# Kernel optimization log

Measured on AMD Instinct MI355X. Metric: run time of the kernel, lower is better.

## Reference

```python
import jax, jax.numpy as jnp
import numpy as np
from jax import lax

B = 32768        # batch
L = 1024         # input_size
K = 5            # kernel_size
PAD = K - 1      # circular padding = 4
FEA = L + (PAD - K // 2) * 2   # mem_fea_dim = 1028
MEM_DIM = 50
DATE_DIM = 32
SHRINK = 0.0025
EPS = 1e-12
DN = ('NCH', 'OIH', 'NCH')


def setup_inputs() -> dict:
    key = jax.random.key(0)
    ks = jax.random.split(key, 10)
    s = 0.05
    return {
        'x': jax.random.normal(ks[0], (B, L), jnp.float32),
        'date_vector': jax.random.normal(ks[1], (B, DATE_DIM), jnp.float32),
        'conv_w': jax.random.normal(ks[2], (1, 1, K), jnp.float32) * s,    # Conv1d weight [out,in,k]
        'convt_w': jax.random.normal(ks[3], (1, 1, K), jnp.float32) * s,   # ConvTranspose1d weight
        'mem_W': jax.random.normal(ks[4], (MEM_DIM, FEA), jnp.float32) * s,      # memory bank (codebook)
        'date_W': jax.random.normal(ks[5], (MEM_DIM, DATE_DIM), jnp.float32) * s, # date addressing weights
        'fcw_w': jax.random.normal(ks[6], (1, L), jnp.float32) * s,
        'fcw_b': jnp.zeros((1,), jnp.float32),
        'fcb_w': jax.random.normal(ks[7], (1, L), jnp.float32) * s,
        'fcb_b': jnp.zeros((1,), jnp.float32),
    }


def _forward(x, date_vector, conv_w, convt_w, mem_W, date_W, fcw_w, fcw_b, fcb_w, fcb_b):
    # --- encode: 1-channel circular conv (bias forced to 0 in original forward) ---
    st = x[:, None, :]                                            # [B,1,L]
    stp = jnp.pad(st, ((0, 0), (0, 0), (PAD, PAD)), mode='wrap')  # circular pad
    st = lax.conv_general_dilated(stp, conv_w, (1,), 'VALID', dimension_numbers=DN)  # [B,1,FEA]

    # --- DateMemoryUnit: date-addressed read with hard shrink + L1 renorm ---
    scores = date_vector @ date_W.T                               # [B,MEM_DIM]
    att = jax.nn.softmax(scores, axis=-1)
    att = jax.nn.relu(att - SHRINK) * att / (jnp.abs(att - SHRINK) + EPS)
    att = att / (jnp.sum(jnp.abs(att), axis=-1, keepdims=True) + EPS)
    st_mem = att @ mem_W                                          # [B,FEA]
    st = st_mem.reshape(B, 1, FEA)

    # --- decode: ConvTranspose1d(k=5, stride=1, padding=4) == VALID conv with flipped kernel ---
    st = lax.conv_general_dilated(st, jnp.flip(convt_w, -1), (1,), 'VALID', dimension_numbers=DN)
    st = st[:, 0, :]                                              # [B,L]

    # --- trend blend ---
    mtf = 0.5
    weight = jnp.tanh(x @ fcw_w.T + fcw_b) * mtf + 1.0            # [B,1]
    bias = jnp.tanh(x @ fcb_w.T + fcb_b) * mtf                    # [B,1]
    st = st * weight + bias
    return st, weight, bias


def reference(x, date_vector, conv_w, convt_w, mem_W, date_W, fcw_w, fcw_b, fcb_w, fcb_b):
    return _forward(x, date_vector, conv_w, convt_w, mem_W, date_W, fcw_w, fcw_b, fcb_w, fcb_b)
```

## Files before the change

### kernel.cpp

```cpp
#include <hip/hip_runtime.h>
#include <hip/hip_bf16.h>

#define BB   32768
#define LL   1024
#define FEA  1028
#define MEM  50
#define DATE 32

typedef float  f32x4  __attribute__((ext_vector_type(4)));
typedef __bf16 bf16x8 __attribute__((ext_vector_type(8)));

__device__ __forceinline__ float wave_max(float v) {
    #pragma unroll
    for (int off = 32; off; off >>= 1) v = fmaxf(v, __shfl_xor(v, off));
    return v;
}
__device__ __forceinline__ float wave_sum(float v) {
    #pragma unroll
    for (int off = 32; off; off >>= 1) v += __shfl_xor(v, off);
    return v;
}
__device__ __forceinline__ float fast_tanh(float v) {
    float e = __expf(2.f * v);
    return 1.f - 2.f / (e + 1.f);
}

__global__ __launch_bounds__(256) void prep_and_wb(
        const float* __restrict__ convt_w,
        const float* __restrict__ mem_W,
        const float* __restrict__ x,
        const float* __restrict__ fcw_w, const float* __restrict__ fcw_b,
        const float* __restrict__ fcb_w, const float* __restrict__ fcb_b,
        __bf16* __restrict__ wc,
        float* __restrict__ out) {
    if (blockIdx.x >= 2048) {
        int idx = (blockIdx.x - 2048) * 256 + threadIdx.x;
        int n = idx >> 6, k = idx & 63;
        float acc = 0.f;
        if (k < MEM) {
            #pragma unroll
            for (int j = 0; j < 5; ++j)
                acc += convt_w[j] * mem_W[k * FEA + n + 4 - j];
        }
        wc[n * 64 + k] = (__bf16)acc;
        return;
    }

    const int lane = threadIdx.x & 63;
    const int wid  = threadIdx.x >> 6;
    const int b0   = blockIdx.x * 16;

    f32x4 wv[4], bv[4];
    #pragma unroll
    for (int c = 0; c < 4; ++c) {
        wv[c] = *(const f32x4*)(fcw_w + c * 256 + lane * 4);
        bv[c] = *(const f32x4*)(fcb_w + c * 256 + lane * 4);
    }
    f32x4 xv[4][4];
    #pragma unroll
    for (int rr = 0; rr < 4; ++rr)
        #pragma unroll
        for (int c = 0; c < 4; ++c)
            xv[rr][c] = *(const f32x4*)(x + (size_t)(b0 + wid * 4 + rr) * LL
                                          + c * 256 + lane * 4);
    float fwb = fcw_b[0], fbb = fcb_b[0];
    #pragma unroll
    for (int rr = 0; rr < 4; ++rr) {
        int r = wid * 4 + rr;
        float aw = 0.f, ab = 0.f;
        #pragma unroll
        for (int c = 0; c < 4; ++c)
            #pragma unroll
            for (int j = 0; j < 4; ++j) {
                aw += xv[rr][c][j] * wv[c][j];
                ab += xv[rr][c][j] * bv[c][j];
            }
        #pragma unroll
        for (int off = 1; off <= 32; off <<= 1) {
            aw += __shfl_xor(aw, off);
            ab += __shfl_xor(ab, off);
        }
        if (lane == 0) {
            out[(size_t)BB * LL + (b0 + r)]      = fast_tanh(aw + fwb) * 0.5f + 1.0f;
            out[(size_t)BB * LL + BB + (b0 + r)] = fast_tanh(ab + fbb) * 0.5f;
        }
    }
}

__global__ __launch_bounds__(256) void memconv_main(
        const float* __restrict__ dv,
        const float* __restrict__ dW,
        const __bf16* __restrict__ wc,
        float* __restrict__ out) {
    __shared__ __bf16 att_s[16 * 72];
    __shared__ float  w_s[16], b_s[16];
    __shared__ float  stage[4][16 * 72];

    const int lane = threadIdx.x & 63;
    const int wid  = threadIdx.x >> 6;
    const int cg   = lane & 15;
    const int kg   = lane >> 4;
    const int b0   = blockIdx.x * 16;

    if (threadIdx.x < 16) {
        w_s[threadIdx.x] = out[(size_t)BB * LL + b0 + threadIdx.x];
        b_s[threadIdx.x] = out[(size_t)BB * LL + BB + b0 + threadIdx.x];
    }

    {
        int m = lane < MEM ? lane : MEM - 1;
        float dwv[DATE];
        const f32x4* dwp = (const f32x4*)(dW + m * DATE);
        #pragma unroll
        for (int c = 0; c < 8; ++c) {
            f32x4 v = dwp[c];
            #pragma unroll
            for (int j = 0; j < 4; ++j) dwv[c * 4 + j] = v[j];
        }
        #pragma unroll
        for (int rr = 0; rr < 4; ++rr) {
            int r = wid * 4 + rr;
            const f32x4* dvp = (const f32x4*)(dv + (size_t)(b0 + r) * DATE);
            float sc = 0.f;
            #pragma unroll
            for (int c = 0; c < 8; ++c) {
                f32x4 v = dvp[c];
                #pragma unroll
                for (int j = 0; j < 4; ++j) sc += v[j] * dwv[c * 4 + j];
            }
            float scm = (lane < MEM) ? sc : -1e30f;
            float mx  = wave_max(scm);
            float e   = (lane < MEM) ? __expf(sc - mx) : 0.f;
            float s   = wave_sum(e);
            float p   = e / s;
            float d   = p - 0.0025f;
            float p2  = (d > 0.f) ? p * d / (d + 1e-12f) : 0.f;
            float s2  = wave_sum(p2) + 1e-12f;
            float att = p2 / s2;
            att_s[r * 72 + lane] = (lane < MEM) ? (__bf16)att : (__bf16)0.f;
        }
    }
    __syncthreads();

    {
        bf16x8 bfr0 = *(const bf16x8*)(att_s + cg * 72 + kg * 8);
        bf16x8 bfr1 = *(const bf16x8*)(att_s + cg * 72 + 32 + kg * 8);
        float* st = stage[wid];
        const int n0 = wid * 256;
        #pragma unroll
        for (int R = 0; R < 4; ++R) {
            #pragma unroll
            for (int t = 0; t < 4; ++t) {
                int n = n0 + (R * 4 + t) * 16 + cg;
                bf16x8 a0 = *(const bf16x8*)(wc + n * 64 + kg * 8);
                bf16x8 a1 = *(const bf16x8*)(wc + n * 64 + 32 + kg * 8);
                f32x4 acc = {0.f, 0.f, 0.f, 0.f};
                acc = __builtin_amdgcn_mfma_f32_16x16x32_bf16(a0, bfr0, acc, 0, 0, 0);
                acc = __builtin_amdgcn_mfma_f32_16x16x32_bf16(a1, bfr1, acc, 0, 0, 0);
                *(f32x4*)(st + cg * 72 + t * 16 + kg * 4) = acc;
            }
            #pragma unroll
            for (int j = 0; j < 4; ++j) {
                int row = j * 4 + (lane >> 4);
                int nl  = (lane & 15) * 4;
                f32x4 v = *(const f32x4*)(st + row * 72 + nl);
                float w = w_s[row], bi = b_s[row];
                f32x4 o;
                #pragma unroll
                for (int k = 0; k < 4; ++k) o[k] = v[k] * w + bi;
                *(f32x4*)(out + (size_t)(b0 + row) * LL + n0 + R * 64 + nl) = o;
            }
        }
    }
}

extern "C" void kernel_launch(void* const* d_in, const int* in_sizes, int n_in,
                              void* d_out, int out_size, void* d_ws, size_t ws_size,
                              hipStream_t stream) {
    const float* x     = (const float*)d_in[0];
    const float* dv    = (const float*)d_in[1];
    const float* convt = (const float*)d_in[3];
    const float* memW  = (const float*)d_in[4];
    const float* dateW = (const float*)d_in[5];
    const float* fcww  = (const float*)d_in[6];
    const float* fcwb  = (const float*)d_in[7];
    const float* fcbw  = (const float*)d_in[8];
    const float* fcbb  = (const float*)d_in[9];
    float* out = (float*)d_out;
    __bf16* wc = (__bf16*)d_ws;

    prep_and_wb <<<2304,    256, 0, stream>>>(convt, memW, x, fcww, fcwb, fcbw, fcbb, wc, out);
    memconv_main<<<BB / 16, 256, 0, stream>>>(dv, dateW, wc, out);
}
```

Measured before the change: 293.3 us.

## Move attention softmax into prep kernel and stream memconv with 32-row blocks

The date-addressed attention (scores, softmax, shrink, renorm) moves out of the main kernel into extra blocks of the prep kernel, which write bf16 attention rows to workspace. The main kernel becomes a pure streaming MFMA+epilogue kernel with no __syncthreads. Each block now covers 32 rows, and each wave handles 16 rows by 512 columns. The per-row weight and bias are broadcast through shuffles instead of shared memory. This adds a small global round trip for the attention values in exchange for a leaner, store-bound main kernel.

```diff
diff --git a/kernel.cpp b/kernel.cpp
--- a/kernel.cpp
+++ b/kernel.cpp
@@ -31,10 +31,16 @@
         const float* __restrict__ x,
         const float* __restrict__ fcw_w, const float* __restrict__ fcw_b,
         const float* __restrict__ fcb_w, const float* __restrict__ fcb_b,
+        const float* __restrict__ dv,
+        const float* __restrict__ dW,
         __bf16* __restrict__ wc,
+        __bf16* __restrict__ att_g,
         float* __restrict__ out) {
-    if (blockIdx.x >= 2048) {
-        int idx = (blockIdx.x - 2048) * 256 + threadIdx.x;
+    const int lane = threadIdx.x & 63;
+    const int wid  = threadIdx.x >> 6;
+
+    if (blockIdx.x >= 4096) {
+        int idx = (blockIdx.x - 4096) * 256 + threadIdx.x;
         int n = idx >> 6, k = idx & 63;
         float acc = 0.f;
         if (k < MEM) {
@@ -46,68 +52,8 @@
         return;
     }
 
-    const int lane = threadIdx.x & 63;
-    const int wid  = threadIdx.x >> 6;
-    const int b0   = blockIdx.x * 16;
-
-    f32x4 wv[4], bv[4];
-    #pragma unroll
-    for (int c = 0; c < 4; ++c) {
-        wv[c] = *(const f32x4*)(fcw_w + c * 256 + lane * 4);
-        bv[c] = *(const f32x4*)(fcb_w + c * 256 + lane * 4);
-    }
-    f32x4 xv[4][4];
-    #pragma unroll
-    for (int rr = 0; rr < 4; ++rr)
-        #pragma unroll
-        for (int c = 0; c < 4; ++c)
-            xv[rr][c] = *(const f32x4*)(x + (size_t)(b0 + wid * 4 + rr) * LL
-                                          + c * 256 + lane * 4);
-    float fwb = fcw_b[0], fbb = fcb_b[0];
-    #pragma unroll
-    for (int rr = 0; rr < 4; ++rr) {
-        int r = wid * 4 + rr;
-        float aw = 0.f, ab = 0.f;
-        #pragma unroll
-        for (int c = 0; c < 4; ++c)
-            #pragma unroll
-            for (int j = 0; j < 4; ++j) {
-                aw += xv[rr][c][j] * wv[c][j];
-                ab += xv[rr][c][j] * bv[c][j];
-            }
-        #pragma unroll
-        for (int off = 1; off <= 32; off <<= 1) {
-            aw += __shfl_xor(aw, off);
-            ab += __shfl_xor(ab, off);
-        }
-        if (lane == 0) {
-            out[(size_t)BB * LL + (b0 + r)]      = fast_tanh(aw + fwb) * 0.5f + 1.0f;
-            out[(size_t)BB * LL + BB + (b0 + r)] = fast_tanh(ab + fbb) * 0.5f;
-        }
-    }
-}
-
-__global__ __launch_bounds__(256) void memconv_main(
-        const float* __restrict__ dv,
-        const float* __restrict__ dW,
-        const __bf16* __restrict__ wc,
-        float* __restrict__ out) {
-    __shared__ __bf16 att_s[16 * 72];
-    __shared__ float  w_s[16], b_s[16];
-    __shared__ float  stage[4][16 * 72];
-
-    const int lane = threadIdx.x & 63;
-    const int wid  = threadIdx.x >> 6;
-    const int cg   = lane & 15;
-    const int kg   = lane >> 4;
-    const int b0   = blockIdx.x * 16;
-
-    if (threadIdx.x < 16) {
-        w_s[threadIdx.x] = out[(size_t)BB * LL + b0 + threadIdx.x];
-        b_s[threadIdx.x] = out[(size_t)BB * LL + BB + b0 + threadIdx.x];
-    }
-
-    {
+    if (blockIdx.x >= 2048) {
+        const int b0 = (blockIdx.x - 2048) * 16;
         int m = lane < MEM ? lane : MEM - 1;
         float dwv[DATE];
         const f32x4* dwp = (const f32x4*)(dW + m * DATE);
@@ -119,8 +65,8 @@
         }
         #pragma unroll
         for (int rr = 0; rr < 4; ++rr) {
-            int r = wid * 4 + rr;
-            const f32x4* dvp = (const f32x4*)(dv + (size_t)(b0 + r) * DATE);
+            int r = b0 + wid * 4 + rr;
+            const f32x4* dvp = (const f32x4*)(dv + (size_t)r * DATE);
             float sc = 0.f;
             #pragma unroll
             for (int c = 0; c < 8; ++c) {
@@ -137,39 +83,99 @@
             float p2  = (d > 0.f) ? p * d / (d + 1e-12f) : 0.f;
             float s2  = wave_sum(p2) + 1e-12f;
             float att = p2 / s2;
-            att_s[r * 72 + lane] = (lane < MEM) ? (__bf16)att : (__bf16)0.f;
-        }
-    }
-    __syncthreads();
-
-    {
-        bf16x8 bfr0 = *(const bf16x8*)(att_s + cg * 72 + kg * 8);
-        bf16x8 bfr1 = *(const bf16x8*)(att_s + cg * 72 + 32 + kg * 8);
-        float* st = stage[wid];
-        const int n0 = wid * 256;
-        #pragma unroll
-        for (int R = 0; R < 4; ++R) {
-            #pragma unroll
-            for (int t = 0; t < 4; ++t) {
-                int n = n0 + (R * 4 + t) * 16 + cg;
-                bf16x8 a0 = *(const bf16x8*)(wc + n * 64 + kg * 8);
-                bf16x8 a1 = *(const bf16x8*)(wc + n * 64 + 32 + kg * 8);
-                f32x4 acc = {0.f, 0.f, 0.f, 0.f};
-                acc = __builtin_amdgcn_mfma_f32_16x16x32_bf16(a0, bfr0, acc, 0, 0, 0);
-                acc = __builtin_amdgcn_mfma_f32_16x16x32_bf16(a1, bfr1, acc, 0, 0, 0);
-                *(f32x4*)(st + cg * 72 + t * 16 + kg * 4) = acc;
+            att_g[(size_t)r * 64 + lane] = (lane < MEM) ? (__bf16)att : (__bf16)0.f;
+        }
+        return;
+    }
+
+    const int b0 = blockIdx.x * 16;
+    f32x4 wv[4], bv[4];
+    #pragma unroll
+    for (int c = 0; c < 4; ++c) {
+        wv[c] = *(const f32x4*)(fcw_w + c * 256 + lane * 4);
+        bv[c] = *(const f32x4*)(fcb_w + c * 256 + lane * 4);
+    }
+    f32x4 xv[4][4];
+    #pragma unroll
+    for (int rr = 0; rr < 4; ++rr)
+        #pragma unroll
+        for (int c = 0; c < 4; ++c)
+            xv[rr][c] = *(const f32x4*)(x + (size_t)(b0 + wid * 4 + rr) * LL
+                                          + c * 256 + lane * 4);
+    float fwb = fcw_b[0], fbb = fcb_b[0];
+    #pragma unroll
+    for (int rr = 0; rr < 4; ++rr) {
+        int r = wid * 4 + rr;
+        float aw = 0.f, ab = 0.f;
+        #pragma unroll
+        for (int c = 0; c < 4; ++c)
+            #pragma unroll
+            for (int j = 0; j < 4; ++j) {
+                aw += xv[rr][c][j] * wv[c][j];
+                ab += xv[rr][c][j] * bv[c][j];
             }
-            #pragma unroll
-            for (int j = 0; j < 4; ++j) {
-                int row = j * 4 + (lane >> 4);
-                int nl  = (lane & 15) * 4;
-                f32x4 v = *(const f32x4*)(st + row * 72 + nl);
-                float w = w_s[row], bi = b_s[row];
-                f32x4 o;
-                #pragma unroll
-                for (int k = 0; k < 4; ++k) o[k] = v[k] * w + bi;
-                *(f32x4*)(out + (size_t)(b0 + row) * LL + n0 + R * 64 + nl) = o;
-            }
+        #pragma unroll
+        for (int off = 1; off <= 32; off <<= 1) {
+            aw += __shfl_xor(aw, off);
+            ab += __shfl_xor(ab, off);
+        }
+        if (lane == 0) {
+            out[(size_t)BB * LL + (b0 + r)]      = fast_tanh(aw + fwb) * 0.5f + 1.0f;
+            out[(size_t)BB * LL + BB + (b0 + r)] = fast_tanh(ab + fbb) * 0.5f;
+        }
+    }
+}
+
+__global__ __launch_bounds__(256) void memconv_stream(
+        const __bf16* __restrict__ wc,
+        const __bf16* __restrict__ att_g,
+        const float* __restrict__ wb,
+        float* __restrict__ out) {
+    __shared__ float stage[4][16 * 72];
+
+    const int lane = threadIdx.x & 63;
+    const int wid  = threadIdx.x >> 6;
+    const int cg   = lane & 15;
+    const int kg   = lane >> 4;
+    const int rg   = wid & 1;
+    const int nh   = wid >> 1;
+    const int r0   = blockIdx.x * 32 + rg * 16;
+    const int n0   = nh * 512;
+
+    bf16x8 bfr0 = *(const bf16x8*)(att_g + (size_t)(r0 + cg) * 64 + kg * 8);
+    bf16x8 bfr1 = *(const bf16x8*)(att_g + (size_t)(r0 + cg) * 64 + 32 + kg * 8);
+
+    float w_reg = wb[r0 + cg];
+    float b_reg = wb[BB + r0 + cg];
+    float wj[4], bj[4];
+    #pragma unroll
+    for (int j = 0; j < 4; ++j) {
+        wj[j] = __shfl(w_reg, j * 4 + kg);
+        bj[j] = __shfl(b_reg, j * 4 + kg);
+    }
+
+    float* st = stage[wid];
+    #pragma unroll 2
+    for (int R = 0; R < 8; ++R) {
+        #pragma unroll
+        for (int t = 0; t < 4; ++t) {
+            int n = n0 + R * 64 + t * 16 + cg;
+            bf16x8 a0 = *(const bf16x8*)(wc + n * 64 + kg * 8);
+            bf16x8 a1 = *(const bf16x8*)(wc + n * 64 + 32 + kg * 8);
+            f32x4 acc = {0.f, 0.f, 0.f, 0.f};
+            acc = __builtin_amdgcn_mfma_f32_16x16x32_bf16(a0, bfr0, acc, 0, 0, 0);
+            acc = __builtin_amdgcn_mfma_f32_16x16x32_bf16(a1, bfr1, acc, 0, 0, 0);
+            *(f32x4*)(st + cg * 72 + t * 16 + kg * 4) = acc;
+        }
+        #pragma unroll
+        for (int j = 0; j < 4; ++j) {
+            int row = j * 4 + kg;
+            int nl  = cg * 4;
+            f32x4 v = *(const f32x4*)(st + row * 72 + nl);
+            f32x4 o;
+            #pragma unroll
+            for (int k = 0; k < 4; ++k) o[k] = v[k] * wj[j] + bj[j];
+            *(f32x4*)(out + (size_t)(r0 + row) * LL + n0 + R * 64 + nl) = o;
         }
     }
 }
@@ -187,8 +193,10 @@
     const float* fcbw  = (const float*)d_in[8];
     const float* fcbb  = (const float*)d_in[9];
     float* out = (float*)d_out;
-    __bf16* wc = (__bf16*)d_ws;
-
-    prep_and_wb <<<2304,    256, 0, stream>>>(convt, memW, x, fcww, fcwb, fcbw, fcbb, wc, out);
-    memconv_main<<<BB / 16, 256, 0, stream>>>(dv, dateW, wc, out);
-}
+    __bf16* wc    = (__bf16*)d_ws;
+    __bf16* att_g = (__bf16*)d_ws + 65536;
+
+    prep_and_wb   <<<4352, 256, 0, stream>>>(convt, memW, x, fcww, fcwb, fcbw, fcbb,
+                                             dv, dateW, wc, att_g, out);
+    memconv_stream<<<BB / 32, 256, 0, stream>>>(wc, att_g, out + (size_t)BB * LL, out);
+}
```

Result: faster. 284.7 us (-2.9%).
